# Performance work log

Measured on AMD Instinct MI355X. Metric: run time of the kernel, lower is better.

The kernel has to match this reference:

```python
import jax, jax.numpy as jnp
import numpy as np


def setup_inputs() -> dict:
    key = jax.random.key(0)
    k1, k2 = jax.random.split(key)
    B, H, W, D, K = 32, 64, 64, 64, 512
    inputs = jax.random.normal(k1, (B, H, W, D), dtype=jnp.float32)
    # codebook: (D, K) as in the keras layer (embedding_dim x num_embeddings)
    embeddings = jax.random.uniform(k2, (D, K), dtype=jnp.float32,
                                    minval=-1.0, maxval=1.0) * (3.0 / D) ** 0.5
    return {"inputs": inputs, "embeddings": embeddings}


def reference(inputs, embeddings):
    # inputs: [B, H, W, D]; embeddings: [D, K]
    D = inputs.shape[-1]
    flat = inputs.reshape(-1, D)                                   # [N, D]
    distances = (jnp.sum(flat * flat, axis=1, keepdims=True)
                 - 2.0 * (flat @ embeddings)
                 + jnp.sum(embeddings * embeddings, axis=0, keepdims=True))
    encoding_indices = jnp.argmin(distances, axis=1)               # [N]
    encoding_indices = encoding_indices.reshape(inputs.shape[:-1])  # [B, H, W]
    quantized = jnp.take(embeddings.T, encoding_indices, axis=0)   # [B, H, W, D]
    # straight-through estimator
    return inputs + jax.lax.stop_gradient(quantized - inputs)
```

## Files before the change

kernel.cpp:

```cpp
#include <hip/hip_runtime.h>


#define KC 512
#define DD 64
#define TAU 5e-4f
#define HTAU (0.5f * TAU)

typedef __attribute__((ext_vector_type(8))) short short8;
typedef __attribute__((ext_vector_type(4))) float float4v;

__device__ inline unsigned short f2bf(float f) {
    unsigned u = __float_as_uint(f);
    return (unsigned short)((u + 0x7FFF + ((u >> 16) & 1)) >> 16);
}
__device__ inline float bf2f(unsigned short b) {
    return __uint_as_float((unsigned)b << 16);
}

__global__ __launch_bounds__(256) void vq_prep(const float* __restrict__ emb,
                                               float* __restrict__ et,
                                               float* __restrict__ bias,
                                               short* __restrict__ Bh,
                                               short* __restrict__ Bl) {
    __shared__ float tile[DD][17];
    const int ct = blockIdx.x;
    const int t  = threadIdx.x;

    {
        const int d = t >> 2, c0 = (t & 3) * 4;
        float4 v = *(const float4*)(emb + (size_t)d * KC + ct * 16 + c0);
        tile[d][c0 + 0] = v.x; tile[d][c0 + 1] = v.y;
        tile[d][c0 + 2] = v.z; tile[d][c0 + 3] = v.w;
    }
    __syncthreads();

    if (t < 16) {
        float s = 0.f;
        #pragma unroll
        for (int d = 0; d < DD; ++d) { float v = tile[d][t]; s += v * v; }
        bias[ct * 16 + t] = s;
    }

    {
        const int c = t >> 4, d0 = (t & 15) * 4;
        float4 v;
        v.x = tile[d0 + 0][c]; v.y = tile[d0 + 1][c];
        v.z = tile[d0 + 2][c]; v.w = tile[d0 + 3][c];
        *(float4*)(et + (size_t)(ct * 16 + c) * DD + d0) = v;
    }

    {
        const int term = t >> 7;
        const int kc   = (t >> 6) & 1;
        const int l    = t & 63;
        const int c    = l & 15, dq = l >> 4;
        short v8[8];
        #pragma unroll
        for (int j = 0; j < 8; ++j) {
            float f = tile[kc * 32 + dq * 8 + j][c];
            unsigned short h = f2bf(f);
            v8[j] = (short)(term == 0 ? h : f2bf(f - bf2f(h)));
        }
        short* dst = (term == 0 ? Bh : Bl) + ((size_t)(ct * 2 + kc) * 64 + l) * 8;
        *(short8*)dst = *(short8*)v8;
    }
}

__global__ __launch_bounds__(512, 2) void vq_main(const float* __restrict__ x_in,
                                                  const short* __restrict__ Bh,
                                                  const short* __restrict__ Bl,
                                                  const float* __restrict__ bias,
                                                  const float* __restrict__ et,
                                                  float* __restrict__ out) {
    __shared__ __align__(16) short Bh_lds[32 * 2 * 64 * 8];
    __shared__ __align__(16) short Bl_lds[32 * 2 * 64 * 8];
    __shared__ float bias_s[KC];
    __shared__ int   k1s[8][64];
    __shared__ float gaps[8][64];

    const int t = threadIdx.x, w = t >> 6, l = t & 63;
    const int col = l & 15, quad = l >> 4;
    const int R0 = blockIdx.x * 512;
    const int wrow0 = w * 64;

    {
        const float4* srcH = (const float4*)Bh;
        const float4* srcL = (const float4*)Bl;
        float4* dstH = (float4*)Bh_lds;
        float4* dstL = (float4*)Bl_lds;
        #pragma unroll
        for (int j = 0; j < 8; ++j) {
            const int idx = t + j * 512;
            dstH[idx] = srcH[idx];
            dstL[idx] = srcL[idx];
        }
        bias_s[t] = bias[t];
    }

    short8 AH[4][2], AL[4][2];
    #pragma unroll
    for (int rt = 0; rt < 4; ++rt)
        #pragma unroll
        for (int kc = 0; kc < 2; ++kc) {
            const float* p = x_in + (size_t)(R0 + wrow0 + rt * 16 + col) * DD
                           + kc * 32 + quad * 8;
            float4 xa = *(const float4*)p;
            float4 xb = *(const float4*)(p + 4);
            float f[8] = {xa.x, xa.y, xa.z, xa.w, xb.x, xb.y, xb.z, xb.w};
            short8 hi8, lo8;
            #pragma unroll
            for (int j = 0; j < 8; ++j) {
                unsigned short h = f2bf(f[j]);
                hi8[j] = (short)h;
                lo8[j] = (short)f2bf(f[j] - bf2f(h));
            }
            AH[rt][kc] = hi8;
            AL[rt][kc] = lo8;
        }
    __syncthreads();

    float m1[4][4], m2[4][4];
    int   kb[4][4];
    #pragma unroll
    for (int rt = 0; rt < 4; ++rt)
        #pragma unroll
        for (int r = 0; r < 4; ++r) {
            m1[rt][r] = -3.4e38f; m2[rt][r] = -3.4e38f; kb[rt][r] = 0;
        }

    #pragma unroll 2
    for (int ct = 0; ct < 32; ++ct) {
        short8 bh0 = *(const short8*)&Bh_lds[((ct * 2 + 0) * 64 + l) * 8];
        short8 bh1 = *(const short8*)&Bh_lds[((ct * 2 + 1) * 64 + l) * 8];
        short8 bl0 = *(const short8*)&Bl_lds[((ct * 2 + 0) * 64 + l) * 8];
        short8 bl1 = *(const short8*)&Bl_lds[((ct * 2 + 1) * 64 + l) * 8];
        const float ci = -0.5f * bias_s[ct * 16 + col];
        const int kk = ct * 16 + col;
        #pragma unroll
        for (int rt = 0; rt < 4; ++rt) {
            float4v c = {ci, ci, ci, ci};
            c = __builtin_amdgcn_mfma_f32_16x16x32_bf16(AH[rt][0], bh0, c, 0, 0, 0);
            c = __builtin_amdgcn_mfma_f32_16x16x32_bf16(AH[rt][1], bh1, c, 0, 0, 0);
            c = __builtin_amdgcn_mfma_f32_16x16x32_bf16(AL[rt][0], bh0, c, 0, 0, 0);
            c = __builtin_amdgcn_mfma_f32_16x16x32_bf16(AL[rt][1], bh1, c, 0, 0, 0);
            c = __builtin_amdgcn_mfma_f32_16x16x32_bf16(AH[rt][0], bl0, c, 0, 0, 0);
            c = __builtin_amdgcn_mfma_f32_16x16x32_bf16(AH[rt][1], bl1, c, 0, 0, 0);
            #pragma unroll
            for (int r = 0; r < 4; ++r) {
                float cr = c[r];
                bool gt = cr > m1[rt][r];
                m2[rt][r] = fmaxf(fminf(cr, m1[rt][r]), m2[rt][r]);
                kb[rt][r] = gt ? kk : kb[rt][r];
                m1[rt][r] = fmaxf(m1[rt][r], cr);
            }
        }
    }

    #pragma unroll
    for (int rt = 0; rt < 4; ++rt)
        #pragma unroll
        for (int r = 0; r < 4; ++r) {
            float b1 = m1[rt][r], b2 = m2[rt][r];
            int   bk = kb[rt][r];
            #pragma unroll
            for (int m = 1; m <= 8; m <<= 1) {
                float o1 = __shfl_xor(b1, m, 64);
                float o2 = __shfl_xor(b2, m, 64);
                int   ok = __shfl_xor(bk, m, 64);
                float n2 = fmaxf(fmaxf(b2, o2), fminf(b1, o1));
                bool take = (o1 > b1) || (o1 == b1 && ok < bk);
                b1 = take ? o1 : b1;
                bk = take ? ok : bk;
                b2 = n2;
            }
            if (col == 0) {
                const int rowl = rt * 16 + quad * 4 + r;
                k1s[w][rowl]  = bk;
                gaps[w][rowl] = b1 - b2;
            }
        }
    __syncthreads();

    {
        unsigned long long mask = __ballot(gaps[w][l] <= HTAU);
        while (mask) {
            const int rr = __builtin_ctzll(mask);
            mask &= mask - 1;
            const size_t grow = (size_t)(R0 + wrow0 + rr) * DD;
            const int kbase = l * 8;
            float acc[8];
            #pragma unroll
            for (int j = 0; j < 8; ++j) acc[j] = 0.f;
            for (int d0 = 0; d0 < DD; d0 += 4) {
                float4 xv = *(const float4*)(x_in + grow + d0);
                #pragma unroll
                for (int j = 0; j < 8; ++j) {
                    float4 ev = *(const float4*)(et + (size_t)(kbase + j) * DD + d0);
                    acc[j] += xv.x * ev.x;
                    acc[j] += xv.y * ev.y;
                    acc[j] += xv.z * ev.z;
                    acc[j] += xv.w * ev.w;
                }
            }
            float4 b0 = *(const float4*)(bias + kbase);
            float4 b1v = *(const float4*)(bias + kbase + 4);
            float bb[8] = {b0.x, b0.y, b0.z, b0.w, b1v.x, b1v.y, b1v.z, b1v.w};
            float bv = 3.4e38f; int bk = 0;
            #pragma unroll
            for (int j = 0; j < 8; ++j) {
                float s = bb[j] - 2.f * acc[j];
                if (s < bv) { bv = s; bk = kbase + j; }
            }
            #pragma unroll
            for (int m = 1; m <= 32; m <<= 1) {
                float ov = __shfl_xor(bv, m, 64);
                int   ok = __shfl_xor(bk, m, 64);
                if (ov < bv || (ov == bv && ok < bk)) { bv = ov; bk = ok; }
            }
            if (l == 0) k1s[w][rr] = bk;
        }
    }

    {
        const int c4 = col * 4;
        #pragma unroll
        for (int i = 0; i < 16; ++i) {
            const int rowl = i * 4 + quad;
            const int bk = k1s[w][rowl];
            float4 v = *(const float4*)(et + (size_t)bk * DD + c4);
            *(float4*)(out + (size_t)(R0 + wrow0 + rowl) * DD + c4) = v;
        }
    }
}

extern "C" void kernel_launch(void* const* d_in, const int* in_sizes, int n_in,
                              void* d_out, int out_size, void* d_ws, size_t ws_size,
                              hipStream_t stream) {
    const float* x_in = (const float*)d_in[0];
    const float* emb  = (const float*)d_in[1];
    float* out = (float*)d_out;

    float* et   = (float*)d_ws;
    float* bias = et + KC * DD;
    short* Bh   = (short*)(bias + KC);
    short* Bl   = Bh + 32 * 2 * 64 * 8;

    const int N = out_size / DD;

    vq_prep<<<32, 256, 0, stream>>>(emb, et, bias, Bh, Bl);
    vq_main<<<N / 512, 512, 0, stream>>>(x_in, Bh, Bl, bias, et, out);
}
```

Before: 126.7 us.

## Switch distance GEMM from 16x16x32 to 32x32x16 bf16 MFMA tiles

Recasts the split-bf16 distance matmul to use 32x32x16 MFMA instructions instead of 16x16x32. The codebook fragment layout in the prep kernel, the A-fragment loads, the per-row argmin state (16 accumulator rows per tile) and the cross-lane reduction all change to match the 32-wide output layout. Larger tiles mean fewer B-fragment LDS reads per MAC and fewer instructions to issue. In exchange, register pressure rises (2x16 min/min2/index state plus a 16-float accumulator), and the reduction shuffle needs one extra step.

```diff
diff --git a/kernel.cpp b/kernel.cpp
--- a/kernel.cpp
+++ b/kernel.cpp
@@ -8,6 +8,7 @@
 
 typedef __attribute__((ext_vector_type(8))) short short8;
 typedef __attribute__((ext_vector_type(4))) float float4v;
+typedef __attribute__((ext_vector_type(16))) float f32x16;
 
 __device__ inline unsigned short f2bf(float f) {
     unsigned u = __float_as_uint(f);
@@ -22,47 +23,57 @@
                                                float* __restrict__ bias,
                                                short* __restrict__ Bh,
                                                short* __restrict__ Bl) {
-    __shared__ float tile[DD][17];
-    const int ct = blockIdx.x;
-    const int t  = threadIdx.x;
-
-    {
-        const int d = t >> 2, c0 = (t & 3) * 4;
-        float4 v = *(const float4*)(emb + (size_t)d * KC + ct * 16 + c0);
-        tile[d][c0 + 0] = v.x; tile[d][c0 + 1] = v.y;
-        tile[d][c0 + 2] = v.z; tile[d][c0 + 3] = v.w;
+    __shared__ float tile[DD][33];
+    const int ctt = blockIdx.x;
+    const int t   = threadIdx.x;
+
+    {
+        const int d = t >> 2, c0 = (t & 3) * 8;
+        float4 v0 = *(const float4*)(emb + (size_t)d * KC + ctt * 32 + c0);
+        float4 v1 = *(const float4*)(emb + (size_t)d * KC + ctt * 32 + c0 + 4);
+        tile[d][c0 + 0] = v0.x; tile[d][c0 + 1] = v0.y;
+        tile[d][c0 + 2] = v0.z; tile[d][c0 + 3] = v0.w;
+        tile[d][c0 + 4] = v1.x; tile[d][c0 + 5] = v1.y;
+        tile[d][c0 + 6] = v1.z; tile[d][c0 + 7] = v1.w;
     }
     __syncthreads();
 
-    if (t < 16) {
+    if (t < 32) {
         float s = 0.f;
         #pragma unroll
         for (int d = 0; d < DD; ++d) { float v = tile[d][t]; s += v * v; }
-        bias[ct * 16 + t] = s;
-    }
-
-    {
-        const int c = t >> 4, d0 = (t & 15) * 4;
-        float4 v;
-        v.x = tile[d0 + 0][c]; v.y = tile[d0 + 1][c];
-        v.z = tile[d0 + 2][c]; v.w = tile[d0 + 3][c];
-        *(float4*)(et + (size_t)(ct * 16 + c) * DD + d0) = v;
-    }
-
-    {
-        const int term = t >> 7;
-        const int kc   = (t >> 6) & 1;
-        const int l    = t & 63;
-        const int c    = l & 15, dq = l >> 4;
-        short v8[8];
-        #pragma unroll
-        for (int j = 0; j < 8; ++j) {
-            float f = tile[kc * 32 + dq * 8 + j][c];
-            unsigned short h = f2bf(f);
-            v8[j] = (short)(term == 0 ? h : f2bf(f - bf2f(h)));
-        }
-        short* dst = (term == 0 ? Bh : Bl) + ((size_t)(ct * 2 + kc) * 64 + l) * 8;
-        *(short8*)dst = *(short8*)v8;
+        bias[ctt * 32 + t] = s;
+    }
+
+    {
+        const int c = t >> 3, d0 = (t & 7) * 8;
+        float4 v0, v1;
+        v0.x = tile[d0 + 0][c]; v0.y = tile[d0 + 1][c];
+        v0.z = tile[d0 + 2][c]; v0.w = tile[d0 + 3][c];
+        v1.x = tile[d0 + 4][c]; v1.y = tile[d0 + 5][c];
+        v1.z = tile[d0 + 6][c]; v1.w = tile[d0 + 7][c];
+        *(float4*)(et + (size_t)(ctt * 32 + c) * DD + d0)     = v0;
+        *(float4*)(et + (size_t)(ctt * 32 + c) * DD + d0 + 4) = v1;
+    }
+
+    {
+        #pragma unroll
+        for (int pass = 0; pass < 2; ++pass) {
+            const int idx  = pass * 256 + t;
+            const int term = idx >> 8;
+            const int kc   = (idx >> 6) & 3;
+            const int l    = idx & 63;
+            const int c    = l & 31, hg = l >> 5;
+            short v8[8];
+            #pragma unroll
+            for (int j = 0; j < 8; ++j) {
+                float f = tile[kc * 16 + hg * 8 + j][c];
+                unsigned short h = f2bf(f);
+                v8[j] = (short)(term == 0 ? h : f2bf(f - bf2f(h)));
+            }
+            short* dst = (term == 0 ? Bh : Bl) + ((size_t)(ctt * 4 + kc) * 64 + l) * 8;
+            *(short8*)dst = *(short8*)v8;
+        }
     }
 }
 
@@ -72,13 +83,14 @@
                                                   const float* __restrict__ bias,
                                                   const float* __restrict__ et,
                                                   float* __restrict__ out) {
-    __shared__ __align__(16) short Bh_lds[32 * 2 * 64 * 8];
-    __shared__ __align__(16) short Bl_lds[32 * 2 * 64 * 8];
+    __shared__ __align__(16) short Bh_lds[16 * 4 * 64 * 8];
+    __shared__ __align__(16) short Bl_lds[16 * 4 * 64 * 8];
     __shared__ float bias_s[KC];
     __shared__ int   k1s[8][64];
     __shared__ float gaps[8][64];
 
     const int t = threadIdx.x, w = t >> 6, l = t & 63;
+    const int c32 = l & 31, hg = l >> 5;
     const int col = l & 15, quad = l >> 4;
     const int R0 = blockIdx.x * 512;
     const int wrow0 = w * 64;
@@ -97,13 +109,13 @@
         bias_s[t] = bias[t];
     }
 
-    short8 AH[4][2], AL[4][2];
+    short8 AH[2][4], AL[2][4];
     #pragma unroll
-    for (int rt = 0; rt < 4; ++rt)
-        #pragma unroll
-        for (int kc = 0; kc < 2; ++kc) {
-            const float* p = x_in + (size_t)(R0 + wrow0 + rt * 16 + col) * DD
-                           + kc * 32 + quad * 8;
+    for (int rt = 0; rt < 2; ++rt)
+        #pragma unroll
+        for (int kc = 0; kc < 4; ++kc) {
+            const float* p = x_in + (size_t)(R0 + wrow0 + rt * 32 + c32) * DD
+                           + kc * 16 + hg * 8;
             float4 xa = *(const float4*)p;
             float4 xb = *(const float4*)(p + 4);
             float f[8] = {xa.x, xa.y, xa.z, xa.w, xb.x, xb.y, xb.z, xb.w};
@@ -119,34 +131,41 @@
         }
     __syncthreads();
 
-    float m1[4][4], m2[4][4];
-    int   kb[4][4];
+    float m1[2][16], m2[2][16];
+    int   kb[2][16];
     #pragma unroll
-    for (int rt = 0; rt < 4; ++rt)
-        #pragma unroll
-        for (int r = 0; r < 4; ++r) {
+    for (int rt = 0; rt < 2; ++rt)
+        #pragma unroll
+        for (int r = 0; r < 16; ++r) {
             m1[rt][r] = -3.4e38f; m2[rt][r] = -3.4e38f; kb[rt][r] = 0;
         }
 
     #pragma unroll 2
-    for (int ct = 0; ct < 32; ++ct) {
-        short8 bh0 = *(const short8*)&Bh_lds[((ct * 2 + 0) * 64 + l) * 8];
-        short8 bh1 = *(const short8*)&Bh_lds[((ct * 2 + 1) * 64 + l) * 8];
-        short8 bl0 = *(const short8*)&Bl_lds[((ct * 2 + 0) * 64 + l) * 8];
-        short8 bl1 = *(const short8*)&Bl_lds[((ct * 2 + 1) * 64 + l) * 8];
-        const float ci = -0.5f * bias_s[ct * 16 + col];
-        const int kk = ct * 16 + col;
-        #pragma unroll
-        for (int rt = 0; rt < 4; ++rt) {
-            float4v c = {ci, ci, ci, ci};
-            c = __builtin_amdgcn_mfma_f32_16x16x32_bf16(AH[rt][0], bh0, c, 0, 0, 0);
-            c = __builtin_amdgcn_mfma_f32_16x16x32_bf16(AH[rt][1], bh1, c, 0, 0, 0);
-            c = __builtin_amdgcn_mfma_f32_16x16x32_bf16(AL[rt][0], bh0, c, 0, 0, 0);
-            c = __builtin_amdgcn_mfma_f32_16x16x32_bf16(AL[rt][1], bh1, c, 0, 0, 0);
-            c = __builtin_amdgcn_mfma_f32_16x16x32_bf16(AH[rt][0], bl0, c, 0, 0, 0);
-            c = __builtin_amdgcn_mfma_f32_16x16x32_bf16(AH[rt][1], bl1, c, 0, 0, 0);
-            #pragma unroll
-            for (int r = 0; r < 4; ++r) {
+    for (int ctt = 0; ctt < 16; ++ctt) {
+        short8 bh[4], bl[4];
+        #pragma unroll
+        for (int kc = 0; kc < 4; ++kc) {
+            bh[kc] = *(const short8*)&Bh_lds[((ctt * 4 + kc) * 64 + l) * 8];
+            bl[kc] = *(const short8*)&Bl_lds[((ctt * 4 + kc) * 64 + l) * 8];
+        }
+        const float ci = -0.5f * bias_s[ctt * 32 + c32];
+        const int kk = ctt * 32 + c32;
+        #pragma unroll
+        for (int rt = 0; rt < 2; ++rt) {
+            f32x16 c;
+            #pragma unroll
+            for (int r = 0; r < 16; ++r) c[r] = ci;
+            #pragma unroll
+            for (int kc = 0; kc < 4; ++kc)
+                c = __builtin_amdgcn_mfma_f32_32x32x16_bf16(AH[rt][kc], bh[kc], c, 0, 0, 0);
+            #pragma unroll
+            for (int kc = 0; kc < 4; ++kc)
+                c = __builtin_amdgcn_mfma_f32_32x32x16_bf16(AL[rt][kc], bh[kc], c, 0, 0, 0);
+            #pragma unroll
+            for (int kc = 0; kc < 4; ++kc)
+                c = __builtin_amdgcn_mfma_f32_32x32x16_bf16(AH[rt][kc], bl[kc], c, 0, 0, 0);
+            #pragma unroll
+            for (int r = 0; r < 16; ++r) {
                 float cr = c[r];
                 bool gt = cr > m1[rt][r];
                 m2[rt][r] = fmaxf(fminf(cr, m1[rt][r]), m2[rt][r]);
@@ -157,13 +176,13 @@
     }
 
     #pragma unroll
-    for (int rt = 0; rt < 4; ++rt)
-        #pragma unroll
-        for (int r = 0; r < 4; ++r) {
+    for (int rt = 0; rt < 2; ++rt)
+        #pragma unroll
+        for (int r = 0; r < 16; ++r) {
             float b1 = m1[rt][r], b2 = m2[rt][r];
             int   bk = kb[rt][r];
             #pragma unroll
-            for (int m = 1; m <= 8; m <<= 1) {
+            for (int m = 1; m <= 16; m <<= 1) {
                 float o1 = __shfl_xor(b1, m, 64);
                 float o2 = __shfl_xor(b2, m, 64);
                 int   ok = __shfl_xor(bk, m, 64);
@@ -173,8 +192,8 @@
                 bk = take ? ok : bk;
                 b2 = n2;
             }
-            if (col == 0) {
-                const int rowl = rt * 16 + quad * 4 + r;
+            if (c32 == 0) {
+                const int rowl = rt * 32 + (r & 3) + 8 * (r >> 2) + 4 * hg;
                 k1s[w][rowl]  = bk;
                 gaps[w][rowl] = b1 - b2;
             }
@@ -243,10 +262,10 @@
     float* et   = (float*)d_ws;
     float* bias = et + KC * DD;
     short* Bh   = (short*)(bias + KC);
-    short* Bl   = Bh + 32 * 2 * 64 * 8;
+    short* Bl   = Bh + 16 * 4 * 64 * 8;
 
     const int N = out_size / DD;
 
-    vq_prep<<<32, 256, 0, stream>>>(emb, et, bias, Bh, Bl);
+    vq_prep<<<16, 256, 0, stream>>>(emb, et, bias, Bh, Bl);
     vq_main<<<N / 512, 512, 0, stream>>>(x_in, Bh, Bl, bias, et, out);
 }
```

After: 140.5 us. 10.9% more time.
